# Kernel optimization log

Hardware: AMD Instinct MI355X
Metric: run time of the kernel (lower is better)

Reference implementation:

```python
import jax, jax.numpy as jnp
import numpy as np

PAD_IDX = 0
NUM_VISITS, MAX_CODES = 16384, 48
VOCAB, DIM, HID = 20000, 128, 128


def setup_inputs() -> dict:
    key = jax.random.key(0)
    ks = jax.random.split(key, 16)
    ids = jax.random.randint(ks[0], (NUM_VISITS, MAX_CODES), 0, VOCAB)
    # guarantee every visit has at least one non-pad code (original returns
    # zeros for empty visits; we simply avoid that degenerate case)
    ids = ids.at[:, 0].set(jnp.maximum(ids[:, 0], 1))
    s = 0.05
    return {
        "ids": ids,
        "emb": jax.random.normal(ks[1], (VOCAB, DIM), jnp.float32) * s,
        "W1": jax.random.normal(ks[2], (DIM, HID), jnp.float32) * s,
        "b1": jnp.zeros((HID,), jnp.float32),
        "W2": jax.random.normal(ks[3], (HID, HID), jnp.float32) * s,
        "b2": jnp.zeros((HID,), jnp.float32),
        "Wa1": jax.random.normal(ks[4], (HID, HID), jnp.float32) * s,
        "ba1": jnp.zeros((HID,), jnp.float32),
        "wa2": jax.random.normal(ks[5], (HID,), jnp.float32) * s,
        "ba2": jnp.zeros((1,), jnp.float32),
        "Wr1": jax.random.normal(ks[6], (HID, HID), jnp.float32) * s,
        "br1": jnp.zeros((HID,), jnp.float32),
        "Wr2": jax.random.normal(ks[7], (HID, DIM), jnp.float32) * s,
        "br2": jnp.zeros((DIM,), jnp.float32),
    }


def reference(ids, emb, W1, b1, W2, b2, Wa1, ba1, wa2, ba2, Wr1, br1, Wr2, br2):
    # ids: [V, C] padded code indices; pad_idx codes are masked out.
    mask = ids != PAD_IDX                              # [V, C]
    x = emb[ids]                                       # [V, C, D]
    # phi: Linear->SiLU->Linear->SiLU
    h = jax.nn.silu(x @ W1 + b1)
    h = jax.nn.silu(h @ W2 + b2)                       # [V, C, H]
    # attention pooling: Linear->Tanh->Linear(1), masked softmax over codes
    a = jnp.tanh(h @ Wa1 + ba1) @ wa2 + ba2[0]         # [V, C]
    a = jnp.where(mask, a, -jnp.inf)
    a = jax.nn.softmax(a, axis=1)                      # pad rows -> weight 0
    h_pool = jnp.einsum("vc,vch->vh", a, h)            # [V, H]
    # rho: Linear->SiLU->Linear
    v = jax.nn.silu(h_pool @ Wr1 + br1) @ Wr2 + br2    # [V, D]
    return v
```

## Files before the change

kernel.cpp:

```cpp
#include <hip/hip_runtime.h>
#include <math.h>


#define DIM 128
#define MT 16
#define XLDP 136

typedef float f32x4 __attribute__((ext_vector_type(4)));
typedef short short8 __attribute__((ext_vector_type(8)));
typedef unsigned short u16x8 __attribute__((ext_vector_type(8)));

#define MFMA(a, b, c) __builtin_amdgcn_mfma_f32_16x16x32_bf16(a, b, c, 0, 0, 0)

__device__ __forceinline__ float fast_rcp(float x) {
  return __builtin_amdgcn_rcpf(x);
}
__device__ __forceinline__ float silu_f(float v) {
  return v * fast_rcp(1.0f + __expf(-v));
}
__device__ __forceinline__ float tanh_f(float v) {
  float t = __expf(2.0f * v);
  return 1.0f - 2.0f * fast_rcp(t + 1.0f);
}

__device__ __forceinline__ unsigned short bf16_hi(float x, float* hif) {
  unsigned u = __builtin_bit_cast(unsigned, x);
  unsigned h = (u + 0x8000u) >> 16;
  *hif = __builtin_bit_cast(float, h << 16);
  return (unsigned short)h;
}
__device__ __forceinline__ unsigned short bf16_rd(float x) {
  unsigned u = __builtin_bit_cast(unsigned, x);
  return (unsigned short)((u + 0x8000u) >> 16);
}
__device__ __forceinline__ unsigned short f2h(float x) {
  return __builtin_bit_cast(unsigned short, (_Float16)x);
}
__device__ __forceinline__ float h2f(unsigned short u) {
  return (float)__builtin_bit_cast(_Float16, u);
}

__global__ __launch_bounds__(256) void prep_wfrags(
    const float* __restrict__ W1, const float* __restrict__ W2,
    const float* __restrict__ Wa1, const float* __restrict__ Wr1,
    const float* __restrict__ Wr2, unsigned short* __restrict__ frags) {
  const int m = blockIdx.x >> 3, chunk = blockIdx.x & 7;
  const float* W = (m == 0) ? W1 : (m == 1) ? W2 : (m == 2) ? Wa1
                  : (m == 3) ? Wr1 : Wr2;
  unsigned short* fh = frags + (size_t)m * 32768;
  unsigned short* fl = fh + 16384;
  const int fid = chunk * 256 + threadIdx.x;
  const int lane = fid & 63, s = (fid >> 6) & 3, t = fid >> 8;
  const int k0 = s * 32 + (lane >> 4) * 8;
  const int n = t * 16 + (lane & 15);
#pragma unroll
  for (int j = 0; j < 8; ++j) {
    float w = W[(size_t)(k0 + j) * DIM + n];
    float hf;
    unsigned short h = bf16_hi(w, &hf);
    fh[fid * 8 + j] = h;
    fl[fid * 8 + j] = bf16_rd(w - hf);
  }
}

__device__ __forceinline__ void stage_bf16(const float* __restrict__ src,
                                           unsigned short (*xh)[XLDP],
                                           unsigned short (*xl)[XLDP],
                                           int tid) {
  const float4* s = (const float4*)src;
#pragma unroll
  for (int tph = 0; tph < 2; ++tph) {
    int idx = tid + tph * 256;
    int r = idx >> 5, c4 = idx & 31;
    float4 v = s[idx];
    float hf;
    ushort4 h, l;
    h.x = bf16_hi(v.x, &hf); l.x = bf16_rd(v.x - hf);
    h.y = bf16_hi(v.y, &hf); l.y = bf16_rd(v.y - hf);
    h.z = bf16_hi(v.z, &hf); l.z = bf16_rd(v.z - hf);
    h.w = bf16_hi(v.w, &hf); l.w = bf16_rd(v.w - hf);
    *(ushort4*)&xh[r][c4 * 4] = h;
    *(ushort4*)&xl[r][c4 * 4] = l;
  }
}

template <int NT>
__device__ __forceinline__ void gemm_frag(const unsigned short (*xh)[XLDP],
                                          const unsigned short (*xl)[XLDP],
                                          const unsigned short* __restrict__ bhp,
                                          const unsigned short* __restrict__ blp,
                                          int tt0, int lane, f32x4 acc[NT]) {
  const int cr = lane & 15, g = lane >> 4;
  short8 ah[4], al[4];
#pragma unroll
  for (int s = 0; s < 4; ++s) {
    ah[s] = *(const short8*)&xh[cr][s * 32 + g * 8];
    al[s] = *(const short8*)&xl[cr][s * 32 + g * 8];
  }
#pragma unroll
  for (int t = 0; t < NT; ++t) {
    short8 bh[4], bl[4];
#pragma unroll
    for (int s = 0; s < 4; ++s) {
      bh[s] = *(const short8*)(bhp +
          ((size_t)((tt0 + t) * 4 + s) * 64 + lane) * 8);
      bl[s] = *(const short8*)(blp +
          ((size_t)((tt0 + t) * 4 + s) * 64 + lane) * 8);
    }
    f32x4 a0 = {0.f, 0.f, 0.f, 0.f}, a1 = {0.f, 0.f, 0.f, 0.f};
#pragma unroll
    for (int s = 0; s < 4; ++s) {
      a0 = MFMA(ah[s], bh[s], a0);
      a1 = MFMA(ah[s], bl[s], a1);
      a1 = MFMA(al[s], bh[s], a1);
    }
    acc[t] = a0 + a1;
  }
}

__global__ __launch_bounds__(256) void vocab_mfma(
    const float* __restrict__ emb, const unsigned short* __restrict__ frags,
    const float* __restrict__ b1, const float* __restrict__ b2,
    const float* __restrict__ ba1, const float* __restrict__ wa2,
    const float* __restrict__ ba2, unsigned short* __restrict__ H2h,
    float* __restrict__ L) {
  __shared__ unsigned short Xh[2][MT][XLDP], Xl[2][MT][XLDP];
  __shared__ float sP[4][MT];
  const int tid = threadIdx.x, wid = tid >> 6, lane = tid & 63;
  const int cr = lane & 15, g = lane >> 4;
  const int m0 = blockIdx.x * MT;

  stage_bf16(emb + (size_t)m0 * DIM, Xh[0], Xl[0], tid);
  __syncthreads();

  f32x4 acc[2];
  gemm_frag<2>(Xh[0], Xl[0], frags, frags + 16384, wid * 2, lane, acc);
#pragma unroll
  for (int t = 0; t < 2; ++t) {
    const int col = (wid * 2 + t) * 16 + cr;
    const float bv = b1[col];
#pragma unroll
    for (int r = 0; r < 4; ++r) {
      float o = silu_f(acc[t][r] + bv);
      float hf;
      Xh[1][g * 4 + r][col] = bf16_hi(o, &hf);
      Xl[1][g * 4 + r][col] = bf16_rd(o - hf);
    }
  }
  __syncthreads();
  gemm_frag<2>(Xh[1], Xl[1], frags + 32768, frags + 32768 + 16384,
               wid * 2, lane, acc);
#pragma unroll
  for (int t = 0; t < 2; ++t) {
    const int col = (wid * 2 + t) * 16 + cr;
    const float bv = b2[col];
#pragma unroll
    for (int r = 0; r < 4; ++r) {
      float o = silu_f(acc[t][r] + bv);
      float hf;
      const int row = g * 4 + r;
      Xh[0][row][col] = bf16_hi(o, &hf);
      Xl[0][row][col] = bf16_rd(o - hf);
      H2h[(size_t)(m0 + row) * DIM + col] = f2h(o);
    }
  }
  __syncthreads();
  gemm_frag<2>(Xh[0], Xl[0], frags + 65536, frags + 65536 + 16384,
               wid * 2, lane, acc);
  {
    float pl[4] = {0.f, 0.f, 0.f, 0.f};
#pragma unroll
    for (int t = 0; t < 2; ++t) {
      const int col = (wid * 2 + t) * 16 + cr;
      const float bav = ba1[col], wav = wa2[col];
#pragma unroll
      for (int r = 0; r < 4; ++r)
        pl[r] = fmaf(tanh_f(acc[t][r] + bav), wav, pl[r]);
    }
#pragma unroll
    for (int r = 0; r < 4; ++r) {
      float p = pl[r];
      p += __shfl_xor(p, 1, 64);
      p += __shfl_xor(p, 2, 64);
      p += __shfl_xor(p, 4, 64);
      p += __shfl_xor(p, 8, 64);
      if (cr == 0) sP[wid][g * 4 + r] = p;
    }
  }
  __syncthreads();
  if (tid < MT)
    L[m0 + tid] = sP[0][tid] + sP[1][tid] + sP[2][tid] + sP[3][tid] + ba2[0];
}

__global__ __launch_bounds__(512) void pool_rho(
    const int* __restrict__ ids, const float* __restrict__ L,
    const unsigned short* __restrict__ H2h,
    const unsigned short* __restrict__ frags,
    const float* __restrict__ br1, const float* __restrict__ br2,
    float* __restrict__ out) {
  __shared__ unsigned short Xh[2][MT][XLDP], Xl[2][MT][XLDP];
  const int tid = threadIdx.x, wid = tid >> 6, lane = tid & 63;
  const int cr = lane & 15, g = lane >> 4;
  const int li = lane & 15;
  const int m0 = blockIdx.x * MT;

#pragma unroll
  for (int k = 0; k < 2; ++k) {
    const int vi = wid * 2 + k;
    const int v = m0 + vi;
    int id = 0;
    float lg = -3.4e38f;
    if (lane < 48) {
      id = ids[(size_t)v * 48 + lane];
      if (id != 0) lg = L[id];
    }
    float mx = lg;
#pragma unroll
    for (int m = 32; m; m >>= 1) mx = fmaxf(mx, __shfl_xor(mx, m, 64));
    float e = (lg > -3.0e38f) ? __expf(lg - mx) : 0.f;
    float s = e;
#pragma unroll
    for (int m = 32; m; m >>= 1) s += __shfl_xor(s, m, 64);
    const float a = e / s;

    float a8[8] = {0.f, 0.f, 0.f, 0.f, 0.f, 0.f, 0.f, 0.f};
#pragma unroll 4
    for (int c = 0; c < 12; ++c) {
      const int cc = 4 * c + g;
      const float ac = __shfl(a, cc, 64);
      const int idc = __shfl(id, cc, 64);
      const u16x8 hv = *(const u16x8*)(H2h + (size_t)idc * DIM + li * 8);
#pragma unroll
      for (int j = 0; j < 8; ++j)
        a8[j] = fmaf(ac, h2f(hv[j]), a8[j]);
    }
#pragma unroll
    for (int j = 0; j < 8; ++j) {
      a8[j] += __shfl_xor(a8[j], 16, 64);
      a8[j] += __shfl_xor(a8[j], 32, 64);
    }
    if (lane < 16) {
      u16x8 hh, hl;
#pragma unroll
      for (int j = 0; j < 8; ++j) {
        float hf;
        hh[j] = bf16_hi(a8[j], &hf);
        hl[j] = bf16_rd(a8[j] - hf);
      }
      *(u16x8*)&Xh[0][vi][li * 8] = hh;
      *(u16x8*)&Xl[0][vi][li * 8] = hl;
    }
  }
  __syncthreads();

  f32x4 acc2[1];
  gemm_frag<1>(Xh[0], Xl[0], frags + 3 * 32768, frags + 3 * 32768 + 16384,
               wid, lane, acc2);
  {
    const int col = wid * 16 + cr;
    const float bv = br1[col];
#pragma unroll
    for (int r = 0; r < 4; ++r) {
      float o = silu_f(acc2[0][r] + bv);
      float hf;
      Xh[1][g * 4 + r][col] = bf16_hi(o, &hf);
      Xl[1][g * 4 + r][col] = bf16_rd(o - hf);
    }
  }
  __syncthreads();
  gemm_frag<1>(Xh[1], Xl[1], frags + 4 * 32768, frags + 4 * 32768 + 16384,
               wid, lane, acc2);
  {
    const int col = wid * 16 + cr;
    const float bv = br2[col];
#pragma unroll
    for (int r = 0; r < 4; ++r)
      out[(size_t)(m0 + g * 4 + r) * DIM + col] = acc2[0][r] + bv;
  }
}

extern "C" void kernel_launch(void* const* d_in, const int* in_sizes, int n_in,
                              void* d_out, int out_size, void* d_ws,
                              size_t ws_size, hipStream_t stream) {
  const int*   ids = (const int*)  d_in[0];
  const float* emb = (const float*)d_in[1];
  const float* W1  = (const float*)d_in[2];
  const float* b1  = (const float*)d_in[3];
  const float* W2  = (const float*)d_in[4];
  const float* b2  = (const float*)d_in[5];
  const float* Wa1 = (const float*)d_in[6];
  const float* ba1 = (const float*)d_in[7];
  const float* wa2 = (const float*)d_in[8];
  const float* ba2 = (const float*)d_in[9];
  const float* Wr1 = (const float*)d_in[10];
  const float* br1 = (const float*)d_in[11];
  const float* Wr2 = (const float*)d_in[12];
  const float* br2 = (const float*)d_in[13];
  float* out = (float*)d_out;

  const int VOCAB = 20000, V = 16384;

  unsigned short* H2h = (unsigned short*)d_ws;
  float* L = (float*)(H2h + (size_t)VOCAB * DIM);
  unsigned short* frags = (unsigned short*)(L + VOCAB);

  prep_wfrags<<<40, 256, 0, stream>>>(W1, W2, Wa1, Wr1, Wr2, frags);
  vocab_mfma<<<VOCAB / MT, 256, 0, stream>>>(emb, frags, b1, b2, ba1, wa2,
                                             ba2, H2h, L);
  pool_rho<<<V / MT, 512, 0, stream>>>(ids, L, H2h, frags, br1, br2, out);
}
```

Baseline: 123.6 us.

## Use 512 threads in vocab kernel with register-resident weight fragments

The vocab-table kernel grows from 4 to 8 waves per 16-row tile, so each wave computes a single 16-column output tile instead of two. All three layers' weight fragments and biases are loaded into registers up front, together with the embedding row, before the first barrier. This aims to hide global-load latency and raise parallelism per tile. In exchange it costs more registers per thread (24 short8 fragments) under a 512x2 launch bound, and adds partial sums to reduce across 8 waves.

```diff
diff --git a/kernel.cpp b/kernel.cpp
--- a/kernel.cpp
+++ b/kernel.cpp
@@ -63,25 +63,36 @@
   }
 }
 
-__device__ __forceinline__ void stage_bf16(const float* __restrict__ src,
-                                           unsigned short (*xh)[XLDP],
-                                           unsigned short (*xl)[XLDP],
-                                           int tid) {
-  const float4* s = (const float4*)src;
-#pragma unroll
-  for (int tph = 0; tph < 2; ++tph) {
-    int idx = tid + tph * 256;
-    int r = idx >> 5, c4 = idx & 31;
-    float4 v = s[idx];
-    float hf;
-    ushort4 h, l;
-    h.x = bf16_hi(v.x, &hf); l.x = bf16_rd(v.x - hf);
-    h.y = bf16_hi(v.y, &hf); l.y = bf16_rd(v.y - hf);
-    h.z = bf16_hi(v.z, &hf); l.z = bf16_rd(v.z - hf);
-    h.w = bf16_hi(v.w, &hf); l.w = bf16_rd(v.w - hf);
-    *(ushort4*)&xh[r][c4 * 4] = h;
-    *(ushort4*)&xl[r][c4 * 4] = l;
-  }
+__device__ __forceinline__ void stage_from_reg(float4 v,
+                                               unsigned short (*xh)[XLDP],
+                                               unsigned short (*xl)[XLDP],
+                                               int tid) {
+  int r = tid >> 5, c4 = tid & 31;
+  float hf;
+  ushort4 h, l;
+  h.x = bf16_hi(v.x, &hf); l.x = bf16_rd(v.x - hf);
+  h.y = bf16_hi(v.y, &hf); l.y = bf16_rd(v.y - hf);
+  h.z = bf16_hi(v.z, &hf); l.z = bf16_rd(v.z - hf);
+  h.w = bf16_hi(v.w, &hf); l.w = bf16_rd(v.w - hf);
+  *(ushort4*)&xh[r][c4 * 4] = h;
+  *(ushort4*)&xl[r][c4 * 4] = l;
+}
+
+__device__ __forceinline__ f32x4 gemm_reg(const unsigned short (*xh)[XLDP],
+                                          const unsigned short (*xl)[XLDP],
+                                          const short8 bh[4],
+                                          const short8 bl[4], int lane) {
+  const int cr = lane & 15, g = lane >> 4;
+  f32x4 a0 = {0.f, 0.f, 0.f, 0.f}, a1 = {0.f, 0.f, 0.f, 0.f};
+#pragma unroll
+  for (int s = 0; s < 4; ++s) {
+    short8 ah = *(const short8*)&xh[cr][s * 32 + g * 8];
+    short8 al = *(const short8*)&xl[cr][s * 32 + g * 8];
+    a0 = MFMA(ah, bh[s], a0);
+    a1 = MFMA(ah, bl[s], a1);
+    a1 = MFMA(al, bh[s], a1);
+  }
+  return a0 + a1;
 }
 
 template <int NT>
@@ -118,45 +129,55 @@
   }
 }
 
-__global__ __launch_bounds__(256) void vocab_mfma(
+__global__ __launch_bounds__(512, 2) void vocab_mfma(
     const float* __restrict__ emb, const unsigned short* __restrict__ frags,
     const float* __restrict__ b1, const float* __restrict__ b2,
     const float* __restrict__ ba1, const float* __restrict__ wa2,
     const float* __restrict__ ba2, unsigned short* __restrict__ H2h,
     float* __restrict__ L) {
   __shared__ unsigned short Xh[2][MT][XLDP], Xl[2][MT][XLDP];
-  __shared__ float sP[4][MT];
+  __shared__ float sP[8][MT];
   const int tid = threadIdx.x, wid = tid >> 6, lane = tid & 63;
   const int cr = lane & 15, g = lane >> 4;
   const int m0 = blockIdx.x * MT;
 
-  stage_bf16(emb + (size_t)m0 * DIM, Xh[0], Xl[0], tid);
-  __syncthreads();
-
-  f32x4 acc[2];
-  gemm_frag<2>(Xh[0], Xl[0], frags, frags + 16384, wid * 2, lane, acc);
-#pragma unroll
-  for (int t = 0; t < 2; ++t) {
-    const int col = (wid * 2 + t) * 16 + cr;
-    const float bv = b1[col];
+  float4 av = ((const float4*)(emb + (size_t)m0 * DIM))[tid];
+
+  short8 B1h[4], B1l[4], B2h[4], B2l[4], B3h[4], B3l[4];
+#pragma unroll
+  for (int s = 0; s < 4; ++s) {
+    const size_t off = ((size_t)(wid * 4 + s) * 64 + lane) * 8;
+    B1h[s] = *(const short8*)(frags + off);
+    B1l[s] = *(const short8*)(frags + 16384 + off);
+    B2h[s] = *(const short8*)(frags + 32768 + off);
+    B2l[s] = *(const short8*)(frags + 32768 + 16384 + off);
+    B3h[s] = *(const short8*)(frags + 65536 + off);
+    B3l[s] = *(const short8*)(frags + 65536 + 16384 + off);
+  }
+
+  const int col = wid * 16 + cr;
+  const float bv1 = b1[col], bv2 = b2[col];
+  const float bav = ba1[col], wav = wa2[col];
+
+  stage_from_reg(av, Xh[0], Xl[0], tid);
+  __syncthreads();
+
+  {
+    f32x4 acc = gemm_reg(Xh[0], Xl[0], B1h, B1l, lane);
 #pragma unroll
     for (int r = 0; r < 4; ++r) {
-      float o = silu_f(acc[t][r] + bv);
+      float o = silu_f(acc[r] + bv1);
       float hf;
       Xh[1][g * 4 + r][col] = bf16_hi(o, &hf);
       Xl[1][g * 4 + r][col] = bf16_rd(o - hf);
     }
   }
   __syncthreads();
-  gemm_frag<2>(Xh[1], Xl[1], frags + 32768, frags + 32768 + 16384,
-               wid * 2, lane, acc);
-#pragma unroll
-  for (int t = 0; t < 2; ++t) {
-    const int col = (wid * 2 + t) * 16 + cr;
-    const float bv = b2[col];
+  {
+    f32x4 acc = gemm_reg(Xh[1], Xl[1], B2h, B2l, lane);
 #pragma unroll
     for (int r = 0; r < 4; ++r) {
-      float o = silu_f(acc[t][r] + bv);
+      float o = silu_f(acc[r] + bv2);
       float hf;
       const int row = g * 4 + r;
       Xh[0][row][col] = bf16_hi(o, &hf);
@@ -165,21 +186,11 @@
     }
   }
   __syncthreads();
-  gemm_frag<2>(Xh[0], Xl[0], frags + 65536, frags + 65536 + 16384,
-               wid * 2, lane, acc);
-  {
-    float pl[4] = {0.f, 0.f, 0.f, 0.f};
-#pragma unroll
-    for (int t = 0; t < 2; ++t) {
-      const int col = (wid * 2 + t) * 16 + cr;
-      const float bav = ba1[col], wav = wa2[col];
-#pragma unroll
-      for (int r = 0; r < 4; ++r)
-        pl[r] = fmaf(tanh_f(acc[t][r] + bav), wav, pl[r]);
-    }
+  {
+    f32x4 acc = gemm_reg(Xh[0], Xl[0], B3h, B3l, lane);
 #pragma unroll
     for (int r = 0; r < 4; ++r) {
-      float p = pl[r];
+      float p = tanh_f(acc[r] + bav) * wav;
       p += __shfl_xor(p, 1, 64);
       p += __shfl_xor(p, 2, 64);
       p += __shfl_xor(p, 4, 64);
@@ -188,8 +199,12 @@
     }
   }
   __syncthreads();
-  if (tid < MT)
-    L[m0 + tid] = sP[0][tid] + sP[1][tid] + sP[2][tid] + sP[3][tid] + ba2[0];
+  if (tid < MT) {
+    float s = ba2[0];
+#pragma unroll
+    for (int w = 0; w < 8; ++w) s += sP[w][tid];
+    L[m0 + tid] = s;
+  }
 }
 
 __global__ __launch_bounds__(512) void pool_rho(
@@ -305,7 +320,7 @@
   unsigned short* frags = (unsigned short*)(L + VOCAB);
 
   prep_wfrags<<<40, 256, 0, stream>>>(W1, W2, Wa1, Wr1, Wr2, frags);
-  vocab_mfma<<<VOCAB / MT, 256, 0, stream>>>(emb, frags, b1, b2, ba1, wa2,
+  vocab_mfma<<<VOCAB / MT, 512, 0, stream>>>(emb, frags, b1, b2, ba1, wa2,
                                              ba2, H2h, L);
   pool_rho<<<V / MT, 512, 0, stream>>>(ids, L, H2h, frags, br1, br2, out);
 }
```

Result: slower. 127.8 us (+3.4%).
